# Optimization experiments

Measured on AMD Instinct MI355X. Metric: run time of the kernel, lower is better.

Reference implementation:

```python
import jax, jax.numpy as jnp
import numpy as np

B, HG, WG = 2, 64, 64
N = HG * WG
C_IN, C_HID, HEADS, C_OUT = 512, 256, 4, 512
NEG_SLOPE = 0.2   # PyG GATv2Conv default negative_slope
LN_EPS = 1e-5


def _grid_edges(h, w):
    """8-neighborhood grid graph, edge_index[0]=source, edge_index[1]=target."""
    nodes = np.arange(h * w).reshape(h, w)
    srcs, dsts = [], []
    for dh in (-1, 0, 1):
        for dw in (-1, 0, 1):
            if dh == 0 and dw == 0:
                continue
            r0, r1 = max(0, -dh), h - max(0, dh)
            c0, c1 = max(0, -dw), w - max(0, dw)
            srcs.append(nodes[r0:r1, c0:c1].ravel())
            dsts.append(nodes[r0 + dh:r1 + dh, c0 + dw:c1 + dw].ravel())
    return np.stack([np.concatenate(srcs), np.concatenate(dsts)]).astype(np.int64)


def setup_inputs() -> dict:
    key = jax.random.key(0)
    ks = iter(jax.random.split(key, 32))

    def p(shape, scale=0.02):
        return jax.random.normal(next(ks), shape, dtype=jnp.float32) * scale

    return {
        "rgb_features": jax.random.normal(next(ks), (B, N, C_IN), dtype=jnp.float32),
        "x_features": jax.random.normal(next(ks), (B, N, C_IN), dtype=jnp.float32),
        "edge_index": jnp.asarray(_grid_edges(HG, WG)),
        # modality_fusion: Linear(2*C_IN, C_HID) + LayerNorm
        "fusion_w": p((C_HID, 2 * C_IN)), "fusion_b": jnp.zeros((C_HID,), jnp.float32),
        "fusion_g": jnp.ones((C_HID,), jnp.float32), "fusion_beta": jnp.zeros((C_HID,), jnp.float32),
        # GATSegmentation.in_proj + norm
        "inproj_w": p((C_HID, C_HID)), "inproj_b": jnp.zeros((C_HID,), jnp.float32),
        "norm_g": jnp.ones((C_HID,), jnp.float32), "norm_b": jnp.zeros((C_HID,), jnp.float32),
        # GATv2Conv layer 0: C_HID -> C_HID, heads=4, concat=True
        "l0_wl": p((HEADS * C_HID, C_HID)), "l0_bl": jnp.zeros((HEADS * C_HID,), jnp.float32),
        "l0_wr": p((HEADS * C_HID, C_HID)), "l0_br": jnp.zeros((HEADS * C_HID,), jnp.float32),
        "l0_att": p((HEADS, C_HID)), "l0_bias": jnp.zeros((HEADS * C_HID,), jnp.float32),
        # GATv2Conv layer 1 (final): 4*C_HID -> C_HID, heads=1, concat=False
        "l1_wl": p((C_HID, HEADS * C_HID)), "l1_bl": jnp.zeros((C_HID,), jnp.float32),
        "l1_wr": p((C_HID, HEADS * C_HID)), "l1_br": jnp.zeros((C_HID,), jnp.float32),
        "l1_att": p((1, C_HID)), "l1_bias": jnp.zeros((C_HID,), jnp.float32),
        # final_proj: 1x1 conv C_HID -> C_OUT
        "fp_w": p((C_OUT, C_HID)), "fp_b": jnp.zeros((C_OUT,), jnp.float32),
    }


def _ln(x, g, b):
    mu = x.mean(-1, keepdims=True)
    v = ((x - mu) ** 2).mean(-1, keepdims=True)
    return (x - mu) * jax.lax.rsqrt(v + LN_EPS) * g + b


def _gatv2(x, src, dst, wl, bl, wr, br, att, bias, concat):
    """PyG GATv2Conv (share_weights=False): gather, leaky_relu logit, segment softmax over
    target neighborhoods, scatter-add aggregation."""
    n = x.shape[0]
    heads, c = att.shape
    xl = (x @ wl.T + bl).reshape(n, heads, c)   # source-side transform (x_j)
    xr = (x @ wr.T + br).reshape(n, heads, c)   # target-side transform (x_i)
    e = jax.nn.leaky_relu(xl[src] + xr[dst], NEG_SLOPE)        # [E, H, C]
    logit = jnp.einsum('ehc,hc->eh', e, att)                   # [E, H]
    m = jax.ops.segment_max(logit, dst, num_segments=n)
    p = jnp.exp(logit - m[dst])
    z = jax.ops.segment_sum(p, dst, num_segments=n)
    alpha = p / z[dst]                                          # softmax per target node
    out = jax.ops.segment_sum(xl[src] * alpha[..., None], dst, num_segments=n)  # [N, H, C]
    out = out.reshape(n, heads * c) if concat else out.mean(axis=1)
    return out + bias


def reference(rgb_features, x_features, edge_index, fusion_w, fusion_b, fusion_g, fusion_beta,
              inproj_w, inproj_b, norm_g, norm_b,
              l0_wl, l0_bl, l0_wr, l0_br, l0_att, l0_bias,
              l1_wl, l1_bl, l1_wr, l1_br, l1_att, l1_bias,
              fp_w, fp_b):
    b, n, _ = rgb_features.shape
    loops = jnp.arange(n, dtype=edge_index.dtype)  # PyG add_self_loops=True
    src = jnp.concatenate([edge_index[0], loops])
    dst = jnp.concatenate([edge_index[1], loops])

    def single(rgb, xm):  # one graph in the batch (original loops over B in Python)
        comb = jnp.concatenate([rgb, xm], axis=-1)                     # [N, 2*C_IN]
        f = jax.nn.relu(_ln(comb @ fusion_w.T + fusion_b, fusion_g, fusion_beta))
        h = jax.nn.relu(_ln(f @ inproj_w.T + inproj_b, norm_g, norm_b))
        h = jax.nn.relu(_gatv2(h, src, dst, l0_wl, l0_bl, l0_wr, l0_br, l0_att, l0_bias, True))
        h = jax.nn.relu(_gatv2(h, src, dst, l1_wl, l1_bl, l1_wr, l1_br, l1_att, l1_bias, False))
        return h                                                        # [N, C_HID]

    nodes = jax.vmap(single)(rgb_features, x_features)                  # [B, N, C_HID]
    img = nodes.reshape(b, HG, WG, C_HID)
    return jnp.einsum('bhwc,oc->bohw', img, fp_w) + fp_b[None, :, None, None]
```

## Files before the change

kernel.cpp:

```cpp
#include <hip/hip_runtime.h>


#define NNODE 4096
#define LN_EPS 1e-5f
#define LOG2E 1.4426950408889634f

typedef _Float16 half8 __attribute__((ext_vector_type(8)));
typedef _Float16 half4 __attribute__((ext_vector_type(4)));
typedef _Float16 h2 __attribute__((ext_vector_type(2)));
typedef float f32x4 __attribute__((ext_vector_type(4)));

__device__ __forceinline__ float wave_reduce_sum(float v) {
    #pragma unroll
    for (int off = 32; off > 0; off >>= 1) v += __shfl_xor(v, off, 64);
    return v;
}

__device__ __forceinline__ void gload_lds16(const void* g, void* l) {
    __builtin_amdgcn_global_load_lds(
        (const __attribute__((address_space(1))) void*)g,
        (__attribute__((address_space(3))) void*)l, 16, 0, 0);
}

template<int N> __device__ __forceinline__ void waitcnt_vm() {
    if constexpr (N <= 0)      asm volatile("s_waitcnt vmcnt(0)" ::: "memory");
    else if constexpr (N == 2) asm volatile("s_waitcnt vmcnt(2)" ::: "memory");
    else if constexpr (N == 3) asm volatile("s_waitcnt vmcnt(3)" ::: "memory");
    else if constexpr (N == 4) asm volatile("s_waitcnt vmcnt(4)" ::: "memory");
    else                       asm volatile("s_waitcnt vmcnt(8)" ::: "memory");
}
template<int N> __device__ __forceinline__ void waitcnt_vm_lgkm() {
    if constexpr (N <= 0)      asm volatile("s_waitcnt vmcnt(0) lgkmcnt(0)" ::: "memory");
    else if constexpr (N == 2) asm volatile("s_waitcnt vmcnt(2) lgkmcnt(0)" ::: "memory");
    else if constexpr (N == 3) asm volatile("s_waitcnt vmcnt(3) lgkmcnt(0)" ::: "memory");
    else                       asm volatile("s_waitcnt vmcnt(4) lgkmcnt(0)" ::: "memory");
}
__device__ __forceinline__ void barrier_raw() {
    asm volatile("s_barrier" ::: "memory");
}

template<int IT, int JT, int OUTMODE>
__global__ __launch_bounds__(256) void gemm3_k(
    const _Float16* __restrict__ A, const _Float16* __restrict__ W,
    const float* __restrict__ bias_lo, const float* __restrict__ bias_hi,
    int nsplit, void* __restrict__ Cout, int K, int N)
{
    constexpr int BM = 32 * IT, BN = 32 * JT;
    constexpr int CA = (BM * 4) / 256;
    constexpr int CB = (BN * 4) / 256;
    constexpr int L = CA + CB;
    __shared__ _Float16 ldsA[3][BM * 32];
    __shared__ _Float16 ldsB[3][BN * 32];

    const int tid = threadIdx.x;
    const int m0 = blockIdx.y * BM, n0 = blockIdx.x * BN;
    const int lane = tid & 63, w = tid >> 6;
    const int fr = lane & 15, kq = lane >> 4;
    const int sq = (kq ^ (fr & 3)) * 8;
    const int wm = (w & 1) * (16 * IT), wn = (w >> 1) * (16 * JT);

    const _Float16* aP[CA]; int aC[CA];
    #pragma unroll
    for (int i = 0; i < CA; ++i) {
        const int c = i * 256 + tid, r = c >> 2, q = (c & 3) ^ (r & 3);
        aP[i] = A + (size_t)(m0 + r) * K + q * 8;
        aC[i] = c * 8;
    }
    const _Float16* bP[CB]; int bC[CB];
    #pragma unroll
    for (int i = 0; i < CB; ++i) {
        const int c = i * 256 + tid, r = c >> 2, q = (c & 3) ^ (r & 3);
        bP[i] = W + (size_t)(n0 + r) * K + q * 8;
        bC[i] = c * 8;
    }

    f32x4 acc[IT][JT] = {};
    const int NT = K >> 5;

    #pragma unroll
    for (int i = 0; i < CA; ++i) gload_lds16(aP[i], &ldsA[0][aC[i]]);
    #pragma unroll
    for (int i = 0; i < CB; ++i) gload_lds16(bP[i], &ldsB[0][bC[i]]);
    #pragma unroll
    for (int i = 0; i < CA; ++i) gload_lds16(aP[i] + 32, &ldsA[1][aC[i]]);
    #pragma unroll
    for (int i = 0; i < CB; ++i) gload_lds16(bP[i] + 32, &ldsB[1][bC[i]]);

    int bi = 0;
    for (int t = 0; t < NT; ++t) {
        if (t + 1 < NT) waitcnt_vm<L>(); else waitcnt_vm<0>();
        barrier_raw();
        if (t + 2 < NT) {
            int nb = bi + 2; if (nb >= 3) nb -= 3;
            const int k2 = (t + 2) << 5;
            #pragma unroll
            for (int i = 0; i < CA; ++i) gload_lds16(aP[i] + k2, &ldsA[nb][aC[i]]);
            #pragma unroll
            for (int i = 0; i < CB; ++i) gload_lds16(bP[i] + k2, &ldsB[nb][bC[i]]);
        }
        half8 af[IT], bf[JT];
        #pragma unroll
        for (int i = 0; i < IT; ++i)
            af[i] = *(const half8*)&ldsA[bi][(wm + i * 16 + fr) * 32 + sq];
        #pragma unroll
        for (int j = 0; j < JT; ++j)
            bf[j] = *(const half8*)&ldsB[bi][(wn + j * 16 + fr) * 32 + sq];
        #pragma unroll
        for (int i = 0; i < IT; ++i)
            #pragma unroll
            for (int j = 0; j < JT; ++j) {
                if (OUTMODE == 1)
                    acc[i][j] = __builtin_amdgcn_mfma_f32_16x16x32_f16(
                        bf[j], af[i], acc[i][j], 0, 0, 0);
                else
                    acc[i][j] = __builtin_amdgcn_mfma_f32_16x16x32_f16(
                        af[i], bf[j], acc[i][j], 0, 0, 0);
            }
        ++bi; if (bi == 3) bi = 0;
    }

    if (OUTMODE == 1) {
        #pragma unroll
        for (int i = 0; i < IT; ++i) {
            const int m = m0 + wm + i * 16 + fr;
            #pragma unroll
            for (int j = 0; j < JT; ++j) {
                const int nb4 = n0 + wn + j * 16 + kq * 4;
                const float* bp = (nb4 < nsplit) ? bias_lo + nb4
                                                 : bias_hi + (nb4 - nsplit);
                const float4 bv = *(const float4*)bp;
                half4 ov = {(_Float16)(acc[i][j][0] + bv.x),
                            (_Float16)(acc[i][j][1] + bv.y),
                            (_Float16)(acc[i][j][2] + bv.z),
                            (_Float16)(acc[i][j][3] + bv.w)};
                *(half4*)((_Float16*)Cout + (size_t)m * N + nb4) = ov;
            }
        }
    } else {
        #pragma unroll
        for (int j = 0; j < JT; ++j) {
            const int col = n0 + wn + j * 16 + fr;
            const float bc = (col < nsplit) ? bias_lo[col] : bias_hi[col - nsplit];
            #pragma unroll
            for (int i = 0; i < IT; ++i) {
                const int mrun = m0 + wm + i * 16 + kq * 4;
                const int b = mrun >> 12, node = mrun & 4095;
                float4 ov = {acc[i][j][0] + bc, acc[i][j][1] + bc,
                             acc[i][j][2] + bc, acc[i][j][3] + bc};
                *(float4*)((float*)Cout + ((size_t)(b * N + col)) * 4096 + node) = ov;
            }
        }
    }
}

__global__ __launch_bounds__(512) void fusion2_k(
    const float* __restrict__ A0, const float* __restrict__ A1,
    const _Float16* __restrict__ W1, const float* __restrict__ b1,
    const float* __restrict__ g1, const float* __restrict__ be1,
    const _Float16* __restrict__ W2, const float* __restrict__ b2,
    const float* __restrict__ g2, const float* __restrict__ be2,
    _Float16* __restrict__ out)
{
    __shared__ _Float16 lA[3][32 * 32];
    __shared__ _Float16 lB[3][256 * 32];
    __shared__ float lC[32 * 260];
    __shared__ _Float16 lH[8 * 1024];

    const int tid = threadIdx.x;
    const int m0 = blockIdx.x * 32;
    const int lane = tid & 63, w = tid >> 6;
    const int fr = lane & 15, kq = lane >> 4;
    const int sq = (kq ^ (fr & 3)) * 8;
    const int wr = (w & 1) * 16, wc = (w >> 1) * 64;
    const bool stager = (tid < 128);

    const _Float16* bP[2]; int bC[2];
    #pragma unroll
    for (int i = 0; i < 2; ++i) {
        const int c = i * 512 + tid, r = c >> 2, q = (c & 3) ^ (r & 3);
        bP[i] = W1 + (size_t)r * 1024 + q * 8;
        bC[i] = c * 8;
    }
    const int ar = tid >> 2, aq = tid & 3;
    const int asw = (ar * 4 + (aq ^ (ar & 3))) * 8;
    float4 p0, p1;
    auto loadA = [&](int k) {
        const int gk = k + aq * 8;
        const float* s = (gk < 512) ? A0 + (size_t)(m0 + ar) * 512 + gk
                                    : A1 + (size_t)(m0 + ar) * 512 + gk - 512;
        p0 = *(const float4*)s;
        p1 = *(const float4*)(s + 4);
    };
    auto writeA = [&](int b) {
        half8 hv = {(_Float16)p0.x, (_Float16)p0.y, (_Float16)p0.z, (_Float16)p0.w,
                    (_Float16)p1.x, (_Float16)p1.y, (_Float16)p1.z, (_Float16)p1.w};
        *(half8*)&lA[b][asw] = hv;
    };

    f32x4 acc[4] = {};

    if (stager) { loadA(0); writeA(0); loadA(32); }
    #pragma unroll
    for (int i = 0; i < 2; ++i) gload_lds16(bP[i], &lB[0][bC[i]]);
    #pragma unroll
    for (int i = 0; i < 2; ++i) gload_lds16(bP[i] + 32, &lB[1][bC[i]]);

    int bi = 0;
    for (int t = 0; t < 32; ++t) {
        if (t + 1 < 32) {
            if (stager) waitcnt_vm_lgkm<4>(); else waitcnt_vm_lgkm<2>();
        } else {
            waitcnt_vm_lgkm<0>();
        }
        barrier_raw();
        int nb1 = bi + 1; if (nb1 >= 3) nb1 -= 3;
        int nb2 = bi + 2; if (nb2 >= 3) nb2 -= 3;
        if (stager && t + 1 < 32) writeA(nb1);
        if (t + 2 < 32) {
            const int k2 = (t + 2) << 5;
            if (stager) loadA(k2);
            #pragma unroll
            for (int i = 0; i < 2; ++i) gload_lds16(bP[i] + k2, &lB[nb2][bC[i]]);
        }
        half8 af = *(const half8*)&lA[bi][(wr + fr) * 32 + sq];
        half8 bf[4];
        #pragma unroll
        for (int j = 0; j < 4; ++j)
            bf[j] = *(const half8*)&lB[bi][(wc + j * 16 + fr) * 32 + sq];
        #pragma unroll
        for (int j = 0; j < 4; ++j)
            acc[j] = __builtin_amdgcn_mfma_f32_16x16x32_f16(af, bf[j], acc[j], 0, 0, 0);
        ++bi; if (bi == 3) bi = 0;
    }

    #pragma unroll
    for (int j = 0; j < 4; ++j) {
        const int col = wc + j * 16 + fr;
        const float bc = b1[col];
        #pragma unroll
        for (int r4 = 0; r4 < 4; ++r4)
            lC[(wr + kq * 4 + r4) * 260 + col] = acc[j][r4] + bc;
    }
    __syncthreads();

    {
        const float4 gv = *(const float4*)(g1 + lane * 4);
        const float4 bv = *(const float4*)(be1 + lane * 4);
        const int t2i = lane >> 3, gq = (lane >> 1) & 3, qo = (lane & 1) * 4;
        #pragma unroll
        for (int rr = 0; rr < 4; ++rr) {
            const int row = w * 4 + rr;
            const float4 v = *(const float4*)&lC[row * 260 + lane * 4];
            float s  = v.x + v.y + v.z + v.w;
            float s2 = v.x * v.x + v.y * v.y + v.z * v.z + v.w * v.w;
            s = wave_reduce_sum(s);
            s2 = wave_reduce_sum(s2);
            const float mu  = s * (1.0f / 256.0f);
            const float var = s2 * (1.0f / 256.0f) - mu * mu;
            const float rs  = rsqrtf(var + LN_EPS);
            half4 o;
            o[0] = (_Float16)fmaxf((v.x - mu) * rs * gv.x + bv.x, 0.f);
            o[1] = (_Float16)fmaxf((v.y - mu) * rs * gv.y + bv.y, 0.f);
            o[2] = (_Float16)fmaxf((v.z - mu) * rs * gv.z + bv.z, 0.f);
            o[3] = (_Float16)fmaxf((v.w - mu) * rs * gv.w + bv.w, 0.f);
            const int qslot = gq ^ (row & 3);
            *(half4*)&lH[t2i * 1024 + (row * 4 + qslot) * 8 + qo] = o;
        }
    }
    __syncthreads();

    const _Float16* b2P[2]; int b2C[2];
    #pragma unroll
    for (int i = 0; i < 2; ++i) {
        const int c = i * 512 + tid, r = c >> 2, q = (c & 3) ^ (r & 3);
        b2P[i] = W2 + (size_t)r * 256 + q * 8;
        b2C[i] = c * 8;
    }
    f32x4 acc2[4] = {};
    #pragma unroll
    for (int i = 0; i < 2; ++i) gload_lds16(b2P[i], &lB[0][b2C[i]]);
    #pragma unroll
    for (int i = 0; i < 2; ++i) gload_lds16(b2P[i] + 32, &lB[1][b2C[i]]);

    int bi2 = 0;
    for (int t2 = 0; t2 < 8; ++t2) {
        if (t2 + 1 < 8) waitcnt_vm<2>(); else waitcnt_vm<0>();
        barrier_raw();
        if (t2 + 2 < 8) {
            int nb = bi2 + 2; if (nb >= 3) nb -= 3;
            const int k2 = (t2 + 2) << 5;
            #pragma unroll
            for (int i = 0; i < 2; ++i) gload_lds16(b2P[i] + k2, &lB[nb][b2C[i]]);
        }
        const half8 af = *(const half8*)
            &lH[t2 * 1024 + ((wr + fr) * 4 + (kq ^ (fr & 3))) * 8];
        half8 bf[4];
        #pragma unroll
        for (int j = 0; j < 4; ++j)
            bf[j] = *(const half8*)&lB[bi2][(wc + j * 16 + fr) * 32 + sq];
        #pragma unroll
        for (int j = 0; j < 4; ++j)
            acc2[j] = __builtin_amdgcn_mfma_f32_16x16x32_f16(af, bf[j], acc2[j], 0, 0, 0);
        ++bi2; if (bi2 == 3) bi2 = 0;
    }

    #pragma unroll
    for (int j = 0; j < 4; ++j) {
        const int col = wc + j * 16 + fr;
        const float bc = b2[col];
        #pragma unroll
        for (int r4 = 0; r4 < 4; ++r4)
            lC[(wr + kq * 4 + r4) * 260 + col] = acc2[j][r4] + bc;
    }
    __syncthreads();

    {
        const float4 gv = *(const float4*)(g2 + lane * 4);
        const float4 bv = *(const float4*)(be2 + lane * 4);
        #pragma unroll
        for (int rr = 0; rr < 4; ++rr) {
            const int row = w * 4 + rr;
            const float4 v = *(const float4*)&lC[row * 260 + lane * 4];
            float s  = v.x + v.y + v.z + v.w;
            float s2 = v.x * v.x + v.y * v.y + v.z * v.z + v.w * v.w;
            s = wave_reduce_sum(s);
            s2 = wave_reduce_sum(s2);
            const float mu  = s * (1.0f / 256.0f);
            const float var = s2 * (1.0f / 256.0f) - mu * mu;
            const float rs  = rsqrtf(var + LN_EPS);
            half4 o;
            o[0] = (_Float16)fmaxf((v.x - mu) * rs * gv.x + bv.x, 0.f);
            o[1] = (_Float16)fmaxf((v.y - mu) * rs * gv.y + bv.y, 0.f);
            o[2] = (_Float16)fmaxf((v.z - mu) * rs * gv.z + bv.z, 0.f);
            o[3] = (_Float16)fmaxf((v.w - mu) * rs * gv.w + bv.w, 0.f);
            *(half4*)(out + (size_t)(m0 + row) * 256 + lane * 4) = o;
        }
    }
}

__device__ __forceinline__ float dot_leaky(const half8 x0, const half8 x1,
    const half8 r0, const half8 r1, const half8 a0, const half8 a1)
{
    const h2 hz = {(_Float16)0.f, (_Float16)0.f};
    const h2 c02 = {(_Float16)0.2f, (_Float16)0.2f};
    h2 p = hz;
    #pragma unroll
    for (int k = 0; k < 4; ++k) {
        h2 e = ((const h2*)&x0)[k] + ((const h2*)&r0)[k];
        h2 t = __builtin_elementwise_fma(
            __builtin_elementwise_min(e, hz), c02,
            __builtin_elementwise_max(e, hz));
        p = __builtin_elementwise_fma(t, ((const h2*)&a0)[k], p);
    }
    #pragma unroll
    for (int k = 0; k < 4; ++k) {
        h2 e = ((const h2*)&x1)[k] + ((const h2*)&r1)[k];
        h2 t = __builtin_elementwise_fma(
            __builtin_elementwise_min(e, hz), c02,
            __builtin_elementwise_max(e, hz));
        p = __builtin_elementwise_fma(t, ((const h2*)&a1)[k], p);
    }
    return (float)p[0] + (float)p[1];
}

template<int HEADS, int LD, int XROFF, int OC>
__global__ __launch_bounds__(256) void gat3_k(
    const _Float16* __restrict__ xlr, const _Float16* __restrict__ att16,
    const float* __restrict__ bias, _Float16* __restrict__ out)
{
    const int tid = threadIdx.x, wv = tid >> 6, lane = tid & 63;
    const int g = lane >> 4, li = lane & 15;
    const int wid = blockIdx.x * 4 + wv;
    const int gi = (HEADS == 4) ? wid : wid * 4 + g;
    const int h  = (HEADS == 4) ? g : 0;
    const int node = gi & (NNODE - 1);
    const int base = gi - node;
    const int r = node >> 6, c = node & 63;
    const int co = h * 256 + li * 16;

    int sidx[9]; float msk[9];
    {
        const int drs[8] = {-1,-1,-1, 0, 0, 1, 1, 1};
        const int dcs[8] = {-1, 0, 1,-1, 1,-1, 0, 1};
        #pragma unroll
        for (int j = 0; j < 8; ++j) {
            const int rr = r + drs[j], cc = c + dcs[j];
            const bool v = ((unsigned)rr < 64u) & ((unsigned)cc < 64u);
            sidx[j] = v ? (rr * 64 + cc) : node;
            msk[j] = v ? 0.f : -1e30f;
        }
        sidx[8] = node; msk[8] = 0.f;
    }

    const _Float16* xp = xlr + (size_t)base * LD + co;
    const half8 xr0 = *(const half8*)(xlr + (size_t)gi * LD + XROFF + co);
    const half8 xr1 = *(const half8*)(xlr + (size_t)gi * LD + XROFF + co + 8);
    const half8 at0 = *(const half8*)(att16 + h * 256 + li * 16);
    const half8 at1 = *(const half8*)(att16 + h * 256 + li * 16 + 8);

    float lg[9];
    #pragma unroll
    for (int j = 0; j < 9; ++j) {
        const half8 x0 = *(const half8*)(xp + (size_t)sidx[j] * LD);
        const half8 x1 = *(const half8*)(xp + (size_t)sidx[j] * LD + 8);
        float pl = dot_leaky(x0, x1, xr0, xr1, at0, at1);
        pl += __shfl_xor(pl, 1, 64);
        pl += __shfl_xor(pl, 2, 64);
        pl += __shfl_xor(pl, 4, 64);
        pl += __shfl_xor(pl, 8, 64);
        lg[j] = pl + msk[j];
    }
    float m = lg[0];
    #pragma unroll
    for (int j = 1; j < 9; ++j) m = fmaxf(m, lg[j]);
    float pj[9], z = 0.f;
    #pragma unroll
    for (int j = 0; j < 9; ++j) { pj[j] = __builtin_amdgcn_exp2f(lg[j] - m); z += pj[j]; }
    const float inv = __builtin_amdgcn_rcpf(z);

    float acc[16];
    #pragma unroll
    for (int k = 0; k < 16; ++k) acc[k] = 0.f;
    #pragma unroll
    for (int j = 0; j < 9; ++j) {
        const half8 x0 = *(const half8*)(xp + (size_t)sidx[j] * LD);
        const half8 x1 = *(const half8*)(xp + (size_t)sidx[j] * LD + 8);
        const float wj = pj[j];
        #pragma unroll
        for (int k = 0; k < 8; ++k) acc[k]     += wj * (float)x0[k];
        #pragma unroll
        for (int k = 0; k < 8; ++k) acc[8 + k] += wj * (float)x1[k];
    }
    float bv[16];
    #pragma unroll
    for (int q = 0; q < 4; ++q) {
        const float4 b4 = *(const float4*)(bias + h * 256 + li * 16 + q * 4);
        bv[q * 4 + 0] = b4.x; bv[q * 4 + 1] = b4.y;
        bv[q * 4 + 2] = b4.z; bv[q * 4 + 3] = b4.w;
    }
    half8 o0, o1;
    #pragma unroll
    for (int k = 0; k < 8; ++k) o0[k] = (_Float16)fmaxf(acc[k] * inv + bv[k], 0.f);
    #pragma unroll
    for (int k = 0; k < 8; ++k) o1[k] = (_Float16)fmaxf(acc[8 + k] * inv + bv[8 + k], 0.f);
    *(half8*)(out + (size_t)gi * OC + co) = o0;
    *(half8*)(out + (size_t)gi * OC + co + 8) = o1;
}

struct WTab {
    const float* src[9];
    int startblk[10];
    int nelem[9];
    int dstoff[9];
    float scale[9];
};

__global__ __launch_bounds__(256) void wconv_k(WTab t, _Float16* __restrict__ dst)
{
    const int b = blockIdx.x;
    int s = 0;
    #pragma unroll
    for (int i = 1; i < 9; ++i) s += (b >= t.startblk[i]);
    const int e0 = (b - t.startblk[s]) * 1024 + threadIdx.x * 4;
    if (e0 >= t.nelem[s]) return;
    const float4 v = *(const float4*)(t.src[s] + e0);
    const float sc = t.scale[s];
    half4 o = {(_Float16)(v.x * sc), (_Float16)(v.y * sc),
               (_Float16)(v.z * sc), (_Float16)(v.w * sc)};
    *(half4*)(dst + t.dstoff[s] + e0) = o;
}

extern "C" void kernel_launch(void* const* d_in, const int* in_sizes, int n_in,
                              void* d_out, int out_size, void* d_ws, size_t ws_size,
                              hipStream_t stream)
{
    const float* rgb       = (const float*)d_in[0];
    const float* xm        = (const float*)d_in[1];
    const float* fusion_w  = (const float*)d_in[3];
    const float* fusion_b  = (const float*)d_in[4];
    const float* fusion_g  = (const float*)d_in[5];
    const float* fusion_be = (const float*)d_in[6];
    const float* inproj_w  = (const float*)d_in[7];
    const float* inproj_b  = (const float*)d_in[8];
    const float* norm_g    = (const float*)d_in[9];
    const float* norm_b    = (const float*)d_in[10];
    const float* l0_wl     = (const float*)d_in[11];
    const float* l0_bl     = (const float*)d_in[12];
    const float* l0_wr     = (const float*)d_in[13];
    const float* l0_br     = (const float*)d_in[14];
    const float* l0_att    = (const float*)d_in[15];
    const float* l0_bias   = (const float*)d_in[16];
    const float* l1_wl     = (const float*)d_in[17];
    const float* l1_bl     = (const float*)d_in[18];
    const float* l1_wr     = (const float*)d_in[19];
    const float* l1_br     = (const float*)d_in[20];
    const float* l1_att    = (const float*)d_in[21];
    const float* l1_bias   = (const float*)d_in[22];
    const float* fp_w      = (const float*)d_in[23];
    const float* fp_b      = (const float*)d_in[24];

    char* ws = (char*)d_ws;
    _Float16* Wf16 = (_Float16*)ws;
    _Float16* H1   = (_Float16*)(ws + 4194304);
    _Float16* XLR0 = (_Float16*)(ws + 8388608);
    _Float16* GO0  = (_Float16*)(ws + 41943040);
    _Float16* XLR1 = (_Float16*)(ws + 58720256);
    _Float16* GO1  = (_Float16*)(ws + 67108864);

    _Float16* w_fus  = Wf16 + 0;
    _Float16* w_inp  = Wf16 + 262144;
    _Float16* w_l0   = Wf16 + 327680;
    _Float16* w_l1   = Wf16 + 851968;
    _Float16* w_fp   = Wf16 + 1376256;
    _Float16* att0_h = Wf16 + 1507328;
    _Float16* att1_h = Wf16 + 1508352;

    const dim3 blk(256);

    WTab t;
    const float* srcs[9] = {fusion_w, inproj_w, l0_wl, l0_wr, l1_wl, l1_wr,
                            fp_w, l0_att, l1_att};
    const int nel[9]  = {262144, 65536, 262144, 262144, 262144, 262144,
                         131072, 1024, 256};
    const int doff[9] = {0, 262144, 327680, 589824, 851968, 1114112,
                         1376256, 1507328, 1508352};
    const int sblk[10] = {0, 256, 320, 576, 832, 1088, 1344, 1472, 1473, 1474};
    for (int i = 0; i < 9; ++i) {
        t.src[i] = srcs[i]; t.nelem[i] = nel[i]; t.dstoff[i] = doff[i];
        t.scale[i] = (i >= 7) ? LOG2E : 1.0f;
    }
    for (int i = 0; i < 10; ++i) t.startblk[i] = sblk[i];
    wconv_k<<<1474, blk, 0, stream>>>(t, Wf16);

    fusion2_k<<<256, 512, 0, stream>>>(
        rgb, xm, w_fus, fusion_b, fusion_g, fusion_be,
        w_inp, inproj_b, norm_g, norm_b, H1);

    gemm3_k<4, 4, 1><<<dim3(16, 64), blk, 0, stream>>>(
        H1, w_l0, l0_bl, l0_br, 1024, XLR0, 256, 2048);
    gat3_k<4, 2048, 1024, 1024><<<2048, blk, 0, stream>>>(
        XLR0, att0_h, l0_bias, GO0);

    gemm3_k<2, 4, 1><<<dim3(4, 128), blk, 0, stream>>>(
        GO0, w_l1, l1_bl, l1_br, 256, XLR1, 1024, 512);
    gat3_k<1, 512, 256, 256><<<512, blk, 0, stream>>>(
        XLR1, att1_h, l1_bias, GO1);

    gemm3_k<2, 4, 2><<<dim3(4, 128), blk, 0, stream>>>(
        GO1, w_fp, fp_b, fp_b, 512, d_out, 256, 512);
}
```

Baseline: 121.2 us.

## Fuse GAT aggregation with following GEMMs and weight conversion into fusion kernel

```diff
diff --git a/kernel.cpp b/kernel.cpp
--- a/kernel.cpp
+++ b/kernel.cpp
@@ -29,11 +29,8 @@
     else if constexpr (N == 4) asm volatile("s_waitcnt vmcnt(4)" ::: "memory");
     else                       asm volatile("s_waitcnt vmcnt(8)" ::: "memory");
 }
-template<int N> __device__ __forceinline__ void waitcnt_vm_lgkm() {
-    if constexpr (N <= 0)      asm volatile("s_waitcnt vmcnt(0) lgkmcnt(0)" ::: "memory");
-    else if constexpr (N == 2) asm volatile("s_waitcnt vmcnt(2) lgkmcnt(0)" ::: "memory");
-    else if constexpr (N == 3) asm volatile("s_waitcnt vmcnt(3) lgkmcnt(0)" ::: "memory");
-    else                       asm volatile("s_waitcnt vmcnt(4) lgkmcnt(0)" ::: "memory");
+__device__ __forceinline__ void lgkm0() {
+    asm volatile("s_waitcnt lgkmcnt(0)" ::: "memory");
 }
 __device__ __forceinline__ void barrier_raw() {
     asm volatile("s_barrier" ::: "memory");
@@ -108,61 +105,64 @@
         #pragma unroll
         for (int i = 0; i < IT; ++i)
             #pragma unroll
-            for (int j = 0; j < JT; ++j) {
-                if (OUTMODE == 1)
-                    acc[i][j] = __builtin_amdgcn_mfma_f32_16x16x32_f16(
-                        bf[j], af[i], acc[i][j], 0, 0, 0);
-                else
-                    acc[i][j] = __builtin_amdgcn_mfma_f32_16x16x32_f16(
-                        af[i], bf[j], acc[i][j], 0, 0, 0);
-            }
+            for (int j = 0; j < JT; ++j)
+                acc[i][j] = __builtin_amdgcn_mfma_f32_16x16x32_f16(
+                    bf[j], af[i], acc[i][j], 0, 0, 0);
         ++bi; if (bi == 3) bi = 0;
     }
 
-    if (OUTMODE == 1) {
-        #pragma unroll
-        for (int i = 0; i < IT; ++i) {
-            const int m = m0 + wm + i * 16 + fr;
-            #pragma unroll
-            for (int j = 0; j < JT; ++j) {
-                const int nb4 = n0 + wn + j * 16 + kq * 4;
-                const float* bp = (nb4 < nsplit) ? bias_lo + nb4
-                                                 : bias_hi + (nb4 - nsplit);
-                const float4 bv = *(const float4*)bp;
-                half4 ov = {(_Float16)(acc[i][j][0] + bv.x),
-                            (_Float16)(acc[i][j][1] + bv.y),
-                            (_Float16)(acc[i][j][2] + bv.z),
-                            (_Float16)(acc[i][j][3] + bv.w)};
-                *(half4*)((_Float16*)Cout + (size_t)m * N + nb4) = ov;
-            }
-        }
-    } else {
+    #pragma unroll
+    for (int i = 0; i < IT; ++i) {
+        const int m = m0 + wm + i * 16 + fr;
         #pragma unroll
         for (int j = 0; j < JT; ++j) {
-            const int col = n0 + wn + j * 16 + fr;
-            const float bc = (col < nsplit) ? bias_lo[col] : bias_hi[col - nsplit];
-            #pragma unroll
-            for (int i = 0; i < IT; ++i) {
-                const int mrun = m0 + wm + i * 16 + kq * 4;
-                const int b = mrun >> 12, node = mrun & 4095;
-                float4 ov = {acc[i][j][0] + bc, acc[i][j][1] + bc,
-                             acc[i][j][2] + bc, acc[i][j][3] + bc};
-                *(float4*)((float*)Cout + ((size_t)(b * N + col)) * 4096 + node) = ov;
-            }
-        }
-    }
-}
-
-__global__ __launch_bounds__(512) void fusion2_k(
+            const int nb4 = n0 + wn + j * 16 + kq * 4;
+            const float* bp = (nb4 < nsplit) ? bias_lo + nb4
+                                             : bias_hi + (nb4 - nsplit);
+            const float4 bv = *(const float4*)bp;
+            half4 ov = {(_Float16)(acc[i][j][0] + bv.x),
+                        (_Float16)(acc[i][j][1] + bv.y),
+                        (_Float16)(acc[i][j][2] + bv.z),
+                        (_Float16)(acc[i][j][3] + bv.w)};
+            *(half4*)((_Float16*)Cout + (size_t)m * N + nb4) = ov;
+        }
+    }
+}
+
+struct ConvTab {
+    const float* src[7];
+    int startblk[8];
+    int nelem[7];
+    int dstoff[7];
+    float scale[7];
+};
+
+__global__ __launch_bounds__(512) void fusion2b_k(
     const float* __restrict__ A0, const float* __restrict__ A1,
-    const _Float16* __restrict__ W1, const float* __restrict__ b1,
+    const float* __restrict__ W1f, const float* __restrict__ b1,
     const float* __restrict__ g1, const float* __restrict__ be1,
-    const _Float16* __restrict__ W2, const float* __restrict__ b2,
+    const float* __restrict__ W2f, const float* __restrict__ b2,
     const float* __restrict__ g2, const float* __restrict__ be2,
-    _Float16* __restrict__ out)
+    _Float16* __restrict__ out, _Float16* __restrict__ wdst, ConvTab ct)
 {
-    __shared__ _Float16 lA[3][32 * 32];
-    __shared__ _Float16 lB[3][256 * 32];
+    if (blockIdx.x >= 256) {
+        const int cid = blockIdx.x - 256;
+        int s = 0;
+        #pragma unroll
+        for (int i = 1; i < 7; ++i) s += (cid >= ct.startblk[i]);
+        const int e0 = (cid - ct.startblk[s]) * 2048 + threadIdx.x * 4;
+        if (e0 < ct.nelem[s]) {
+            const float4 v = *(const float4*)(ct.src[s] + e0);
+            const float sc = ct.scale[s];
+            half4 o = {(_Float16)(v.x * sc), (_Float16)(v.y * sc),
+                       (_Float16)(v.z * sc), (_Float16)(v.w * sc)};
+            *(half4*)(wdst + ct.dstoff[s] + e0) = o;
+        }
+        return;
+    }
+
+    __shared__ _Float16 lA[2][32 * 32];
+    __shared__ _Float16 lB[2][256 * 32];
     __shared__ float lC[32 * 260];
     __shared__ _Float16 lH[8 * 1024];
 
@@ -174,63 +174,58 @@
     const int wr = (w & 1) * 16, wc = (w >> 1) * 64;
     const bool stager = (tid < 128);
 
-    const _Float16* bP[2]; int bC[2];
-    #pragma unroll
-    for (int i = 0; i < 2; ++i) {
-        const int c = i * 512 + tid, r = c >> 2, q = (c & 3) ^ (r & 3);
-        bP[i] = W1 + (size_t)r * 1024 + q * 8;
-        bC[i] = c * 8;
-    }
+    const int br_ = tid >> 3, bf_ = tid & 7;
+    const int bq_ = bf_ >> 1, bo_ = bf_ & 1;
+    float4 pb[4];
+
     const int ar = tid >> 2, aq = tid & 3;
     const int asw = (ar * 4 + (aq ^ (ar & 3))) * 8;
-    float4 p0, p1;
+    float4 pa0, pa1;
+
+    auto loadB = [&](const float* Wf, int ldw, int k0) {
+        #pragma unroll
+        for (int i = 0; i < 4; ++i)
+            pb[i] = *(const float4*)(Wf + (size_t)(br_ + i * 64) * ldw + k0 + bf_ * 4);
+    };
+    auto writeB = [&](int buf) {
+        #pragma unroll
+        for (int i = 0; i < 4; ++i) {
+            const int r = br_ + i * 64;
+            half4 o = {(_Float16)pb[i].x, (_Float16)pb[i].y,
+                       (_Float16)pb[i].z, (_Float16)pb[i].w};
+            *(half4*)&lB[buf][(r * 4 + (bq_ ^ (r & 3))) * 8 + bo_ * 4] = o;
+        }
+    };
     auto loadA = [&](int k) {
         const int gk = k + aq * 8;
         const float* s = (gk < 512) ? A0 + (size_t)(m0 + ar) * 512 + gk
                                     : A1 + (size_t)(m0 + ar) * 512 + gk - 512;
-        p0 = *(const float4*)s;
-        p1 = *(const float4*)(s + 4);
+        pa0 = *(const float4*)s;
+        pa1 = *(const float4*)(s + 4);
     };
-    auto writeA = [&](int b) {
-        half8 hv = {(_Float16)p0.x, (_Float16)p0.y, (_Float16)p0.z, (_Float16)p0.w,
-                    (_Float16)p1.x, (_Float16)p1.y, (_Float16)p1.z, (_Float16)p1.w};
-        *(half8*)&lA[b][asw] = hv;
+    auto writeA = [&](int buf) {
+        half8 hv = {(_Float16)pa0.x, (_Float16)pa0.y, (_Float16)pa0.z, (_Float16)pa0.w,
+                    (_Float16)pa1.x, (_Float16)pa1.y, (_Float16)pa1.z, (_Float16)pa1.w};
+        *(half8*)&lA[buf][asw] = hv;
     };
 
-    f32x4 acc[4] = {};
-
+    f32x4 acc1[4] = {};
     if (stager) { loadA(0); writeA(0); loadA(32); }
-    #pragma unroll
-    for (int i = 0; i < 2; ++i) gload_lds16(bP[i], &lB[0][bC[i]]);
-    #pragma unroll
-    for (int i = 0; i < 2; ++i) gload_lds16(bP[i] + 32, &lB[1][bC[i]]);
-
-    int bi = 0;
+    loadB(W1f, 1024, 0); writeB(0); loadB(W1f, 1024, 32);
+    lgkm0(); barrier_raw();
     for (int t = 0; t < 32; ++t) {
-        if (t + 1 < 32) {
-            if (stager) waitcnt_vm_lgkm<4>(); else waitcnt_vm_lgkm<2>();
-        } else {
-            waitcnt_vm_lgkm<0>();
-        }
-        barrier_raw();
-        int nb1 = bi + 1; if (nb1 >= 3) nb1 -= 3;
-        int nb2 = bi + 2; if (nb2 >= 3) nb2 -= 3;
-        if (stager && t + 1 < 32) writeA(nb1);
-        if (t + 2 < 32) {
-            const int k2 = (t + 2) << 5;
-            if (stager) loadA(k2);
-            #pragma unroll
-            for (int i = 0; i < 2; ++i) gload_lds16(bP[i] + k2, &lB[nb2][bC[i]]);
-        }
-        half8 af = *(const half8*)&lA[bi][(wr + fr) * 32 + sq];
-        half8 bf[4];
+        if (t + 1 < 32) { writeB((t + 1) & 1); if (stager) writeA((t + 1) & 1); }
+        lgkm0(); barrier_raw();
+        if (t + 2 < 32) { loadB(W1f, 1024, (t + 2) * 32); if (stager) loadA((t + 2) * 32); }
+        const half8 af = *(const half8*)&lA[t & 1][(wr + fr) * 32 + sq];
+        half8 bfr[4];
         #pragma unroll
         for (int j = 0; j < 4; ++j)
-            bf[j] = *(const half8*)&lB[bi][(wc + j * 16 + fr) * 32 + sq];
+            bfr[j] = *(const half8*)&lB[t & 1][(wc + j * 16 + fr) * 32 + sq];
         #pragma unroll
         for (int j = 0; j < 4; ++j)
-            acc[j] = __builtin_amdgcn_mfma_f32_16x16x32_f16(af, bf[j], acc[j], 0, 0, 0);
-        ++bi; if (bi == 3) bi = 0;
+            acc1[j] = __builtin_amdgcn_mfma_f32_16x16x32_f16(af, bfr[j], acc1[j], 0, 0, 0);
+        lgkm0(); barrier_raw();
     }
 
     #pragma unroll
@@ -239,7 +234,7 @@
         const float bc = b1[col];
         #pragma unroll
         for (int r4 = 0; r4 < 4; ++r4)
-            lC[(wr + kq * 4 + r4) * 260 + col] = acc[j][r4] + bc;
+            lC[(wr + kq * 4 + r4) * 260 + col] = acc1[j][r4] + bc;
     }
     __syncthreads();
 
@@ -269,39 +264,23 @@
     }
     __syncthreads();
 
-    const _Float16* b2P[2]; int b2C[2];
-    #pragma unroll
-    for (int i = 0; i < 2; ++i) {
-        const int c = i * 512 + tid, r = c >> 2, q = (c & 3) ^ (r & 3);
-        b2P[i] = W2 + (size_t)r * 256 + q * 8;
-        b2C[i] = c * 8;
-    }
     f32x4 acc2[4] = {};
-    #pragma unroll
-    for (int i = 0; i < 2; ++i) gload_lds16(b2P[i], &lB[0][b2C[i]]);
-    #pragma unroll
-    for (int i = 0; i < 2; ++i) gload_lds16(b2P[i] + 32, &lB[1][b2C[i]]);
-
-    int bi2 = 0;
-    for (int t2 = 0; t2 < 8; ++t2) {
-        if (t2 + 1 < 8) waitcnt_vm<2>(); else waitcnt_vm<0>();
-        barrier_raw();
-        if (t2 + 2 < 8) {
-            int nb = bi2 + 2; if (nb >= 3) nb -= 3;
-            const int k2 = (t2 + 2) << 5;
-            #pragma unroll
-            for (int i = 0; i < 2; ++i) gload_lds16(b2P[i] + k2, &lB[nb][b2C[i]]);
-        }
+    loadB(W2f, 256, 0); writeB(0); loadB(W2f, 256, 32);
+    lgkm0(); barrier_raw();
+    for (int t = 0; t < 8; ++t) {
+        if (t + 1 < 8) writeB((t + 1) & 1);
+        lgkm0(); barrier_raw();
+        if (t + 2 < 8) loadB(W2f, 256, (t + 2) * 32);
         const half8 af = *(const half8*)
-            &lH[t2 * 1024 + ((wr + fr) * 4 + (kq ^ (fr & 3))) * 8];
-        half8 bf[4];
+            &lH[t * 1024 + ((wr + fr) * 4 + (kq ^ (fr & 3))) * 8];
+        half8 bfr[4];
         #pragma unroll
         for (int j = 0; j < 4; ++j)
-            bf[j] = *(const half8*)&lB[bi2][(wc + j * 16 + fr) * 32 + sq];
+            bfr[j] = *(const half8*)&lB[t & 1][(wc + j * 16 + fr) * 32 + sq];
         #pragma unroll
         for (int j = 0; j < 4; ++j)
-            acc2[j] = __builtin_amdgcn_mfma_f32_16x16x32_f16(af, bf[j], acc2[j], 0, 0, 0);
-        ++bi2; if (bi2 == 3) bi2 = 0;
+            acc2[j] = __builtin_amdgcn_mfma_f32_16x16x32_f16(af, bfr[j], acc2[j], 0, 0, 0);
+        lgkm0(); barrier_raw();
     }
 
     #pragma unroll
@@ -338,136 +317,199 @@
     }
 }
 
-__device__ __forceinline__ float dot_leaky(const half8 x0, const half8 x1,
-    const half8 r0, const half8 r1, const half8 a0, const half8 a1)
+template<int HEADS, int K, int LD, int XROFF, int OUTMODE>
+__global__ __launch_bounds__(512) void gatgemm_k(
+    const _Float16* __restrict__ xlr, const _Float16* __restrict__ att16,
+    const float* __restrict__ gbias, const _Float16* __restrict__ W,
+    const float* __restrict__ bias_lo, const float* __restrict__ bias_hi,
+    int nsplit, void* __restrict__ Cout)
 {
-    const h2 hz = {(_Float16)0.f, (_Float16)0.f};
-    const h2 c02 = {(_Float16)0.2f, (_Float16)0.2f};
-    h2 p = hz;
-    #pragma unroll
-    for (int k = 0; k < 4; ++k) {
-        h2 e = ((const h2*)&x0)[k] + ((const h2*)&r0)[k];
-        h2 t = __builtin_elementwise_fma(
-            __builtin_elementwise_min(e, hz), c02,
-            __builtin_elementwise_max(e, hz));
-        p = __builtin_elementwise_fma(t, ((const h2*)&a0)[k], p);
-    }
-    #pragma unroll
-    for (int k = 0; k < 4; ++k) {
-        h2 e = ((const h2*)&x1)[k] + ((const h2*)&r1)[k];
-        h2 t = __builtin_elementwise_fma(
-            __builtin_elementwise_min(e, hz), c02,
-            __builtin_elementwise_max(e, hz));
-        p = __builtin_elementwise_fma(t, ((const h2*)&a1)[k], p);
-    }
-    return (float)p[0] + (float)p[1];
-}
-
-template<int HEADS, int LD, int XROFF, int OC>
-__global__ __launch_bounds__(256) void gat3_k(
-    const _Float16* __restrict__ xlr, const _Float16* __restrict__ att16,
-    const float* __restrict__ bias, _Float16* __restrict__ out)
-{
-    const int tid = threadIdx.x, wv = tid >> 6, lane = tid & 63;
+    constexpr int PAD = K + 8;
+    constexpr int NT = K / 32;
+    __shared__ _Float16 lA[32 * PAD];
+    __shared__ _Float16 lB[2][512 * 32];
+
+    const int tid = threadIdx.x;
+    const int m0 = blockIdx.x * 32;
+    const int lane = tid & 63, w = tid >> 6;
     const int g = lane >> 4, li = lane & 15;
-    const int wid = blockIdx.x * 4 + wv;
-    const int gi = (HEADS == 4) ? wid : wid * 4 + g;
-    const int h  = (HEADS == 4) ? g : 0;
-    const int node = gi & (NNODE - 1);
-    const int base = gi - node;
-    const int r = node >> 6, c = node & 63;
-    const int co = h * 256 + li * 16;
-
-    int sidx[9]; float msk[9];
-    {
-        const int drs[8] = {-1,-1,-1, 0, 0, 1, 1, 1};
-        const int dcs[8] = {-1, 0, 1,-1, 1,-1, 0, 1};
-        #pragma unroll
-        for (int j = 0; j < 8; ++j) {
-            const int rr = r + drs[j], cc = c + dcs[j];
-            const bool v = ((unsigned)rr < 64u) & ((unsigned)cc < 64u);
-            sidx[j] = v ? (rr * 64 + cc) : node;
-            msk[j] = v ? 0.f : -1e30f;
-        }
-        sidx[8] = node; msk[8] = 0.f;
-    }
-
-    const _Float16* xp = xlr + (size_t)base * LD + co;
-    const half8 xr0 = *(const half8*)(xlr + (size_t)gi * LD + XROFF + co);
-    const half8 xr1 = *(const half8*)(xlr + (size_t)gi * LD + XROFF + co + 8);
-    const half8 at0 = *(const half8*)(att16 + h * 256 + li * 16);
-    const half8 at1 = *(const half8*)(att16 + h * 256 + li * 16 + 8);
-
-    float lg[9];
-    #pragma unroll
-    for (int j = 0; j < 9; ++j) {
-        const half8 x0 = *(const half8*)(xp + (size_t)sidx[j] * LD);
-        const half8 x1 = *(const half8*)(xp + (size_t)sidx[j] * LD + 8);
-        float pl = dot_leaky(x0, x1, xr0, xr1, at0, at1);
-        pl += __shfl_xor(pl, 1, 64);
-        pl += __shfl_xor(pl, 2, 64);
-        pl += __shfl_xor(pl, 4, 64);
-        pl += __shfl_xor(pl, 8, 64);
-        lg[j] = pl + msk[j];
-    }
-    float m = lg[0];
-    #pragma unroll
-    for (int j = 1; j < 9; ++j) m = fmaxf(m, lg[j]);
-    float pj[9], z = 0.f;
-    #pragma unroll
-    for (int j = 0; j < 9; ++j) { pj[j] = __builtin_amdgcn_exp2f(lg[j] - m); z += pj[j]; }
-    const float inv = __builtin_amdgcn_rcpf(z);
-
-    float acc[16];
-    #pragma unroll
-    for (int k = 0; k < 16; ++k) acc[k] = 0.f;
-    #pragma unroll
-    for (int j = 0; j < 9; ++j) {
-        const half8 x0 = *(const half8*)(xp + (size_t)sidx[j] * LD);
-        const half8 x1 = *(const half8*)(xp + (size_t)sidx[j] * LD + 8);
-        const float wj = pj[j];
-        #pragma unroll
-        for (int k = 0; k < 8; ++k) acc[k]     += wj * (float)x0[k];
-        #pragma unroll
-        for (int k = 0; k < 8; ++k) acc[8 + k] += wj * (float)x1[k];
-    }
-    float bv[16];
-    #pragma unroll
-    for (int q = 0; q < 4; ++q) {
-        const float4 b4 = *(const float4*)(bias + h * 256 + li * 16 + q * 4);
-        bv[q * 4 + 0] = b4.x; bv[q * 4 + 1] = b4.y;
-        bv[q * 4 + 2] = b4.z; bv[q * 4 + 3] = b4.w;
-    }
-    half8 o0, o1;
-    #pragma unroll
-    for (int k = 0; k < 8; ++k) o0[k] = (_Float16)fmaxf(acc[k] * inv + bv[k], 0.f);
-    #pragma unroll
-    for (int k = 0; k < 8; ++k) o1[k] = (_Float16)fmaxf(acc[8 + k] * inv + bv[8 + k], 0.f);
-    *(half8*)(out + (size_t)gi * OC + co) = o0;
-    *(half8*)(out + (size_t)gi * OC + co + 8) = o1;
-}
-
-struct WTab {
-    const float* src[9];
-    int startblk[10];
-    int nelem[9];
-    int dstoff[9];
-    float scale[9];
-};
-
-__global__ __launch_bounds__(256) void wconv_k(WTab t, _Float16* __restrict__ dst)
-{
-    const int b = blockIdx.x;
-    int s = 0;
-    #pragma unroll
-    for (int i = 1; i < 9; ++i) s += (b >= t.startblk[i]);
-    const int e0 = (b - t.startblk[s]) * 1024 + threadIdx.x * 4;
-    if (e0 >= t.nelem[s]) return;
-    const float4 v = *(const float4*)(t.src[s] + e0);
-    const float sc = t.scale[s];
-    half4 o = {(_Float16)(v.x * sc), (_Float16)(v.y * sc),
-               (_Float16)(v.z * sc), (_Float16)(v.w * sc)};
-    *(half4*)(dst + t.dstoff[s] + e0) = o;
+
+    const _Float16* bP[4]; int bC[4];
+    #pragma unroll
+    for (int i = 0; i < 4; ++i) {
+        const int c = i * 512 + tid, r = c >> 2, q = (c & 3) ^ (r & 3);
+        bP[i] = W + (size_t)r * K + q * 8;
+        bC[i] = c * 8;
+    }
+    #pragma unroll
+    for (int i = 0; i < 4; ++i) gload_lds16(bP[i], &lB[0][bC[i]]);
+    #pragma unroll
+    for (int i = 0; i < 4; ++i) gload_lds16(bP[i] + 32, &lB[1][bC[i]]);
+
+    const int rounds = (HEADS == 4) ? 4 : 1;
+    for (int rr = 0; rr < rounds; ++rr) {
+        const int row = (HEADS == 4) ? (w * 4 + rr) : (w * 4 + g);
+        const int gi = m0 + row;
+        const int node = gi & (NNODE - 1);
+        const int base = gi - node;
+        const int h = (HEADS == 4) ? g : 0;
+        const int nr = node >> 6, nc = node & 63;
+        const int co = h * 256 + li * 16;
+
+        int sidx[9]; float msk[9];
+        {
+            const int drs[8] = {-1,-1,-1, 0, 0, 1, 1, 1};
+            const int dcs[8] = {-1, 0, 1,-1, 1,-1, 0, 1};
+            #pragma unroll
+            for (int j = 0; j < 8; ++j) {
+                const int rj = nr + drs[j], cj = nc + dcs[j];
+                const bool v = ((unsigned)rj < 64u) & ((unsigned)cj < 64u);
+                sidx[j] = v ? (rj * 64 + cj) : node;
+                msk[j] = v ? 0.f : -1e30f;
+            }
+            sidx[8] = node; msk[8] = 0.f;
+        }
+        const _Float16* xp = xlr + (size_t)base * LD + co;
+        const half8 xr0 = *(const half8*)(xlr + (size_t)gi * LD + XROFF + co);
+        const half8 xr1 = *(const half8*)(xlr + (size_t)gi * LD + XROFF + co + 8);
+        const half8 at0 = *(const half8*)(att16 + h * 256 + li * 16);
+        const half8 at1 = *(const half8*)(att16 + h * 256 + li * 16 + 8);
+        const h2 hz = {(_Float16)0.f, (_Float16)0.f};
+        const h2 c02 = {(_Float16)0.2f, (_Float16)0.2f};
+
+        float lg[9];
+        #pragma unroll
+        for (int j = 0; j < 9; ++j) {
+            const half8 x0 = *(const half8*)(xp + (size_t)sidx[j] * LD);
+            const half8 x1 = *(const half8*)(xp + (size_t)sidx[j] * LD + 8);
+            h2 p = hz;
+            #pragma unroll
+            for (int k = 0; k < 4; ++k) {
+                h2 e = ((const h2*)&x0)[k] + ((const h2*)&xr0)[k];
+                h2 tt = __builtin_elementwise_fma(
+                    __builtin_elementwise_min(e, hz), c02,
+                    __builtin_elementwise_max(e, hz));
+                p = __builtin_elementwise_fma(tt, ((const h2*)&at0)[k], p);
+            }
+            #pragma unroll
+            for (int k = 0; k < 4; ++k) {
+                h2 e = ((const h2*)&x1)[k] + ((const h2*)&xr1)[k];
+                h2 tt = __builtin_elementwise_fma(
+                    __builtin_elementwise_min(e, hz), c02,
+                    __builtin_elementwise_max(e, hz));
+                p = __builtin_elementwise_fma(tt, ((const h2*)&at1)[k], p);
+            }
+            float pl = (float)p[0] + (float)p[1];
+            pl += __shfl_xor(pl, 1, 64);
+            pl += __shfl_xor(pl, 2, 64);
+            pl += __shfl_xor(pl, 4, 64);
+            pl += __shfl_xor(pl, 8, 64);
+            lg[j] = pl + msk[j];
+        }
+        float m = lg[0];
+        #pragma unroll
+        for (int j = 1; j < 9; ++j) m = fmaxf(m, lg[j]);
+        float pj[9], z = 0.f;
+        #pragma unroll
+        for (int j = 0; j < 9; ++j) { pj[j] = __builtin_amdgcn_exp2f(lg[j] - m); z += pj[j]; }
+        const float inv = __builtin_amdgcn_rcpf(z);
+
+        float acc[16];
+        #pragma unroll
+        for (int k = 0; k < 16; ++k) acc[k] = 0.f;
+        #pragma unroll
+        for (int j = 0; j < 9; ++j) {
+            const half8 x0 = *(const half8*)(xp + (size_t)sidx[j] * LD);
+            const half8 x1 = *(const half8*)(xp + (size_t)sidx[j] * LD + 8);
+            const float wj = pj[j];
+            #pragma unroll
+            for (int k = 0; k < 8; ++k) acc[k]     += wj * (float)x0[k];
+            #pragma unroll
+            for (int k = 0; k < 8; ++k) acc[8 + k] += wj * (float)x1[k];
+        }
+        float bv[16];
+        #pragma unroll
+        for (int q = 0; q < 4; ++q) {
+            const float4 b4 = *(const float4*)(gbias + h * 256 + li * 16 + q * 4);
+            bv[q * 4 + 0] = b4.x; bv[q * 4 + 1] = b4.y;
+            bv[q * 4 + 2] = b4.z; bv[q * 4 + 3] = b4.w;
+        }
+        half8 o0, o1;
+        #pragma unroll
+        for (int k = 0; k < 8; ++k) o0[k] = (_Float16)fmaxf(acc[k] * inv + bv[k], 0.f);
+        #pragma unroll
+        for (int k = 0; k < 8; ++k) o1[k] = (_Float16)fmaxf(acc[8 + k] * inv + bv[8 + k], 0.f);
+        *(half8*)&lA[row * PAD + co] = o0;
+        *(half8*)&lA[row * PAD + co + 8] = o1;
+    }
+    __syncthreads();
+
+    const int fr = lane & 15, kq = lane >> 4;
+    const int sq = (kq ^ (fr & 3)) * 8;
+    const int wc = w * 64;
+    f32x4 acc[2][4] = {};
+
+    for (int t = 0; t < NT; ++t) {
+        if (t + 1 < NT) waitcnt_vm<4>(); else waitcnt_vm<0>();
+        barrier_raw();
+        half8 af[2]; half8 bfr[4];
+        #pragma unroll
+        for (int i = 0; i < 2; ++i)
+            af[i] = *(const half8*)&lA[(i * 16 + fr) * PAD + t * 32 + kq * 8];
+        #pragma unroll
+        for (int j = 0; j < 4; ++j)
+            bfr[j] = *(const half8*)&lB[t & 1][(wc + j * 16 + fr) * 32 + sq];
+        lgkm0(); barrier_raw();
+        if (t + 2 < NT) {
+            #pragma unroll
+            for (int i = 0; i < 4; ++i)
+                gload_lds16(bP[i] + (t + 2) * 32, &lB[t & 1][bC[i]]);
+        }
+        #pragma unroll
+        for (int i = 0; i < 2; ++i)
+            #pragma unroll
+            for (int j = 0; j < 4; ++j) {
+                if (OUTMODE == 1)
+                    acc[i][j] = __builtin_amdgcn_mfma_f32_16x16x32_f16(
+                        bfr[j], af[i], acc[i][j], 0, 0, 0);
+                else
+                    acc[i][j] = __builtin_amdgcn_mfma_f32_16x16x32_f16(
+                        af[i], bfr[j], acc[i][j], 0, 0, 0);
+            }
+    }
+
+    if (OUTMODE == 1) {
+        #pragma unroll
+        for (int i = 0; i < 2; ++i) {
+            const int m = m0 + i * 16 + fr;
+            #pragma unroll
+            for (int j = 0; j < 4; ++j) {
+                const int nb4 = wc + j * 16 + kq * 4;
+                const float* bp = (nb4 < nsplit) ? bias_lo + nb4
+                                                 : bias_hi + (nb4 - nsplit);
+                const float4 bvv = *(const float4*)bp;
+                half4 ov = {(_Float16)(acc[i][j][0] + bvv.x),
+                            (_Float16)(acc[i][j][1] + bvv.y),
+                            (_Float16)(acc[i][j][2] + bvv.z),
+                            (_Float16)(acc[i][j][3] + bvv.w)};
+                *(half4*)((_Float16*)Cout + (size_t)m * 512 + nb4) = ov;
+            }
+        }
+    } else {
+        #pragma unroll
+        for (int j = 0; j < 4; ++j) {
+            const int col = wc + j * 16 + fr;
+            const float bc = bias_lo[col];
+            #pragma unroll
+            for (int i = 0; i < 2; ++i) {
+                const int mrun = m0 + i * 16 + kq * 4;
+                const int b = mrun >> 12, node = mrun & 4095;
+                float4 ov = {acc[i][j][0] + bc, acc[i][j][1] + bc,
+                             acc[i][j][2] + bc, acc[i][j][3] + bc};
+                *(float4*)((float*)Cout + ((size_t)(b * 512 + col)) * 4096 + node) = ov;
+            }
+        }
+    }
 }
 
 extern "C" void kernel_launch(void* const* d_in, const int* in_sizes, int n_in,
@@ -503,49 +545,35 @@
     _Float16* Wf16 = (_Float16*)ws;
     _Float16* H1   = (_Float16*)(ws + 4194304);
     _Float16* XLR0 = (_Float16*)(ws + 8388608);
-    _Float16* GO0  = (_Float16*)(ws + 41943040);
-    _Float16* XLR1 = (_Float16*)(ws + 58720256);
-    _Float16* GO1  = (_Float16*)(ws + 67108864);
-
-    _Float16* w_fus  = Wf16 + 0;
-    _Float16* w_inp  = Wf16 + 262144;
+    _Float16* XLR1 = (_Float16*)(ws + 41943040);
+
     _Float16* w_l0   = Wf16 + 327680;
     _Float16* w_l1   = Wf16 + 851968;
     _Float16* w_fp   = Wf16 + 1376256;
     _Float16* att0_h = Wf16 + 1507328;
     _Float16* att1_h = Wf16 + 1508352;
 
-    const dim3 blk(256);
-
-    WTab t;
-    const float* srcs[9] = {fusion_w, inproj_w, l0_wl, l0_wr, l1_wl, l1_wr,
-                            fp_w, l0_att, l1_att};
-    const int nel[9]  = {262144, 65536, 262144, 262144, 262144, 262144,
-                         131072, 1024, 256};
-    const int doff[9] = {0, 262144, 327680, 589824, 851968, 1114112,
-                         1376256, 1507328, 1508352};
-    const int sblk[10] = {0, 256, 320, 576, 832, 1088, 1344, 1472, 1473, 1474};
-    for (int i = 0; i < 9; ++i) {
-        t.src[i] = srcs[i]; t.nelem[i] = nel[i]; t.dstoff[i] = doff[i];
-        t.scale[i] = (i >= 7) ? LOG2E : 1.0f;
-    }
-    for (int i = 0; i < 10; ++i) t.startblk[i] = sblk[i];
-    wconv_k<<<1474, blk, 0, stream>>>(t, Wf16);
-
-    fusion2_k<<<256, 512, 0, stream>>>(
-        rgb, xm, w_fus, fusion_b, fusion_g, fusion_be,
-        w_inp, inproj_b, norm_g, norm_b, H1);
-
-    gemm3_k<4, 4, 1><<<dim3(16, 64), blk, 0, stream>>>(
+    ConvTab ct;
+    const float* srcs[7] = {l0_wl, l0_wr, l1_wl, l1_wr, fp_w, l0_att, l1_att};
+    const int nel[7]  = {262144, 262144, 262144, 262144, 131072, 1024, 256};
+    const int doff[7] = {327680, 589824, 851968, 1114112, 1376256, 1507328, 1508352};
+    const int sblk[8] = {0, 128, 256, 384, 512, 576, 577, 578};
+    for (int i = 0; i < 7; ++i) {
+        ct.src[i] = srcs[i]; ct.nelem[i] = nel[i]; ct.dstoff[i] = doff[i];
+        ct.scale[i] = (i >= 5) ? LOG2E : 1.0f;
+    }
+    for (int i = 0; i < 8; ++i) ct.startblk[i] = sblk[i];
+
+    fusion2b_k<<<834, 512, 0, stream>>>(
+        rgb, xm, fusion_w, fusion_b, fusion_g, fusion_be,
+        inproj_w, inproj_b, norm_g, norm_b, H1, Wf16, ct);
+
+    gemm3_k<4, 4, 1><<<dim3(16, 64), 256, 0, stream>>>(
         H1, w_l0, l0_bl, l0_br, 1024, XLR0, 256, 2048);
-    gat3_k<4, 2048, 1024, 1024><<<2048, blk, 0, stream>>>(
-        XLR0, att0_h, l0_bias, GO0);
-
-    gemm3_k<2, 4, 1><<<dim3(4, 128), blk, 0, stream>>>(
-        GO0, w_l1, l1_bl, l1_br, 256, XLR1, 1024, 512);
-    gat3_k<1, 512, 256, 256><<<512, blk, 0, stream>>>(
-        XLR1, att1_h, l1_bias, GO1);
-
-    gemm3_k<2, 4, 2><<<dim3(4, 128), blk, 0, stream>>>(
-        GO1, w_fp, fp_b, fp_b, 512, d_out, 256, 512);
-}
+
+    gatgemm_k<4, 1024, 2048, 1024, 1><<<256, 512, 0, stream>>>(
+        XLR0, att0_h, l0_bias, w_l1, l1_bl, l1_br, 256, XLR1);
+
+    gatgemm_k<1, 256, 512, 256, 2><<<256, 512, 0, stream>>>(
+        XLR1, att1_h, l1_bias, w_fp, fp_b, fp_b, 512, d_out);
+}
```

Result: slower. 127.3 us (+5.0%).
